# Optimization experiments

Hardware: AMD Instinct MI355X
Metric: run time of the kernel (lower is better)

Reference implementation:

```python
import jax, jax.numpy as jnp
import numpy as np

NUM_HEAD = 16
DIM = 1024
T, B = 2048, 4


def setup_inputs() -> dict:
    key = jax.random.key(0)
    ks = jax.random.split(key, 12)
    s = 1.0 / np.sqrt(DIM)
    return {
        "x1": jax.random.normal(ks[0], (T, B, DIM), jnp.float32),
        "x2": jax.random.normal(ks[1], (T, B, DIM), jnp.float32),
        "Wq": jax.random.normal(ks[2], (DIM, DIM), jnp.float32) * s,
        "bq": jax.random.normal(ks[3], (DIM,), jnp.float32) * 0.01,
        "Wk": jax.random.normal(ks[4], (DIM, DIM), jnp.float32) * s,
        "bk": jax.random.normal(ks[5], (DIM,), jnp.float32) * 0.01,
        "Wv": jax.random.normal(ks[6], (DIM, DIM), jnp.float32) * s,
        "bv": jax.random.normal(ks[7], (DIM,), jnp.float32) * 0.01,
        "Wu": jax.random.normal(ks[8], (DIM, DIM), jnp.float32) * s,
        "bu": jax.random.normal(ks[9], (DIM,), jnp.float32) * 0.01,
    }


def reference(x1, x2, Wq, bq, Wk, bk, Wv, bv, Wu, bu):
    T1, B1, C = x1.shape
    T2 = x2.shape[0]
    H = NUM_HEAD
    hd = C // H
    # (T,B,C) -> (B,T,C)
    x1b = jnp.transpose(x1, (1, 0, 2))
    x2b = jnp.transpose(x2, (1, 0, 2))
    # torch Linear: y = x @ W.T + b
    q = (x1b @ Wq.T + bq).reshape(B1, T1, H, hd).transpose(0, 2, 1, 3)  # (B,H,T1,hd)
    k = (x2b @ Wk.T + bk).reshape(B1, T2, H, hd).transpose(0, 2, 1, 3)
    v = (x2b @ Wv.T + bv).reshape(B1, T2, H, hd).transpose(0, 2, 1, 3)
    # NOTE: source scales by 1/sqrt(C) (full dim), not 1/sqrt(head_dim)
    attn = jnp.einsum("bhqd,bhkd->bhqk", q, k) / jnp.sqrt(jnp.asarray(C, q.dtype))
    attn = jax.nn.softmax(attn, axis=-1)
    # dropout = identity (eval mode, deterministic reference)
    out = jnp.einsum("bhqk,bhkd->bhqd", attn, v)  # (B,H,T1,hd)
    out = out.transpose(0, 2, 1, 3).reshape(B1, T1, C)  # merge heads
    out = out @ Wu.T + bu
    return out
```

## Files before the change

### kernel.cpp

```cpp
#include <hip/hip_runtime.h>

#define TSEQ 2048
#define BB 4
#define CDIM 1024
#define NH 16
#define HD 64
#define MR (TSEQ*BB)
#define C2SCALE 0.045084220f

typedef __attribute__((ext_vector_type(8))) short sh8;
typedef __attribute__((ext_vector_type(4))) short sh4;
typedef __attribute__((ext_vector_type(4))) float f4;

__device__ __forceinline__ unsigned short f2bf(float x){
  unsigned u = __builtin_bit_cast(unsigned, x);
  u += 0x7fffu + ((u>>16)&1u);
  return (unsigned short)(u>>16);
}

__device__ __forceinline__ unsigned pk2(float a, float b){
  unsigned ua = __builtin_bit_cast(unsigned, a) + 0x8000u;
  unsigned ub = __builtin_bit_cast(unsigned, b) + 0x8000u;
  return __builtin_amdgcn_perm(ua, ub, 0x07060302u);
}

__device__ __forceinline__ void gll16(const unsigned short* g, unsigned short* l){
  __builtin_amdgcn_global_load_lds(
      (const __attribute__((address_space(1))) unsigned int*)g,
      (__attribute__((address_space(3))) unsigned int*)l, 16, 0, 0);
}

__global__ void conv_x(const float* __restrict__ a, const float* __restrict__ b,
                       unsigned short* __restrict__ ya, unsigned short* __restrict__ yb){
  const float* s = blockIdx.y ? b : a;
  unsigned short* d = blockIdx.y ? yb : ya;
  int i = (blockIdx.x*256 + threadIdx.x)*4;
  f4 v = *(const f4*)(s+i);
  sh4 o;
  o.x = (short)f2bf(v.x); o.y = (short)f2bf(v.y);
  o.z = (short)f2bf(v.z); o.w = (short)f2bf(v.w);
  *(sh4*)(d+i) = o;
}

__global__ void conv_w(const float* __restrict__ w0, const float* __restrict__ w1,
                       const float* __restrict__ w2, const float* __restrict__ w3,
                       unsigned short* __restrict__ y0, unsigned short* __restrict__ y1,
                       unsigned short* __restrict__ y2, unsigned short* __restrict__ y3){
  const float* s; unsigned short* d;
  switch(blockIdx.y){
    case 0: s=w0; d=y0; break;
    case 1: s=w1; d=y1; break;
    case 2: s=w2; d=y2; break;
    default: s=w3; d=y3; break;
  }
  int i = (blockIdx.x*256 + threadIdx.x)*4;
  f4 v = *(const f4*)(s+i);
  sh4 o;
  o.x = (short)f2bf(v.x); o.y = (short)f2bf(v.y);
  o.z = (short)f2bf(v.z); o.w = (short)f2bf(v.w);
  *(sh4*)(d+i) = o;
}

template<int MODE>
__global__ __launch_bounds__(256,2) void gemm_bt(
    const unsigned short* __restrict__ A, const unsigned short* __restrict__ Bw,
    const float* __restrict__ bias, void* __restrict__ Cout){
  __shared__ unsigned short As[128*32];
  __shared__ unsigned short Bs[128*32];
  const int tid  = threadIdx.x;
  const int wave = tid>>6, lane = tid&63;
  const int g = lane>>4, c = lane&15;
  const int m0 = blockIdx.x*128, n0 = blockIdx.y*128;
  const int wr = wave>>1, wc = wave&1;
  f4 acc[4][4] = {};
  const int r0 = tid>>2, cc0 = tid&3;
  const unsigned short* Ag = A  + (size_t)(m0+r0)*CDIM + cc0*8;
  const unsigned short* Bg = Bw + (size_t)(n0+r0)*CDIM + cc0*8;

  for (int k0=0; k0<CDIM; k0+=32){
    __syncthreads();
    gll16(Ag + k0,                    As + tid*8);
    gll16(Ag + (size_t)64*CDIM + k0,  As + (256+tid)*8);
    gll16(Bg + k0,                    Bs + tid*8);
    gll16(Bg + (size_t)64*CDIM + k0,  Bs + (256+tid)*8);
    __syncthreads();
    sh8 af[4], bfr[4];
#pragma unroll
    for (int mt=0; mt<4; mt++) af[mt]  = *(const sh8*)(As + (wr*64+mt*16+c)*32 + g*8);
#pragma unroll
    for (int nt=0; nt<4; nt++) bfr[nt] = *(const sh8*)(Bs + (wc*64+nt*16+c)*32 + g*8);
#pragma unroll
    for (int mt=0; mt<4; mt++)
#pragma unroll
      for (int nt=0; nt<4; nt++)
        acc[mt][nt] = __builtin_amdgcn_mfma_f32_16x16x32_bf16(af[mt], bfr[nt], acc[mt][nt], 0,0,0);
  }

#pragma unroll
  for (int nt=0; nt<4; nt++){
    int nn = n0 + wc*64 + nt*16 + c;
    float bsv = bias[nn];
#pragma unroll
    for (int mt=0; mt<4; mt++){
      int mb = m0 + wr*64 + mt*16 + 4*g;
#pragma unroll
      for (int r=0; r<4; r++){
        float v = acc[mt][nt][r] + bsv;
        int mm = mb + r;
        if (MODE==3){
          ((unsigned short*)Cout)[(size_t)mm*CDIM + nn] = f2bf(v*C2SCALE);
        } else {
          ((float*)Cout)[(size_t)mm*CDIM + nn] = v;
        }
      }
    }
  }
}

__global__ __launch_bounds__(256,2) void gemm_kv(
    const unsigned short* __restrict__ A,
    const unsigned short* __restrict__ Bk, const unsigned short* __restrict__ Bv,
    const float* __restrict__ biask, const float* __restrict__ biasv,
    unsigned short* __restrict__ Kout, unsigned short* __restrict__ Vout){
  __shared__ unsigned short As[128*32];
  __shared__ unsigned short Bs1[128*32];
  __shared__ unsigned short Bs2[128*32];
  const int tid  = threadIdx.x;
  const int wave = tid>>6, lane = tid&63;
  const int g = lane>>4, c = lane&15;
  const int m0 = blockIdx.x*128, n0 = blockIdx.y*128;
  const int wr = wave>>1, wc = wave&1;
  f4 acck[4][4] = {}, accv[4][4] = {};
  const int r0 = tid>>2, cc0 = tid&3;
  const unsigned short* Ag  = A  + (size_t)(m0+r0)*CDIM + cc0*8;
  const unsigned short* Bkg = Bk + (size_t)(n0+r0)*CDIM + cc0*8;
  const unsigned short* Bvg = Bv + (size_t)(n0+r0)*CDIM + cc0*8;

  for (int k0=0; k0<CDIM; k0+=32){
    __syncthreads();
    gll16(Ag  + k0,                    As  + tid*8);
    gll16(Ag  + (size_t)64*CDIM + k0,  As  + (256+tid)*8);
    gll16(Bkg + k0,                    Bs1 + tid*8);
    gll16(Bkg + (size_t)64*CDIM + k0,  Bs1 + (256+tid)*8);
    gll16(Bvg + k0,                    Bs2 + tid*8);
    gll16(Bvg + (size_t)64*CDIM + k0,  Bs2 + (256+tid)*8);
    __syncthreads();
    sh8 af[4], bk4[4], bv4[4];
#pragma unroll
    for (int mt=0; mt<4; mt++) af[mt]  = *(const sh8*)(As  + (wr*64+mt*16+c)*32 + g*8);
#pragma unroll
    for (int nt=0; nt<4; nt++) bk4[nt] = *(const sh8*)(Bs1 + (wc*64+nt*16+c)*32 + g*8);
#pragma unroll
    for (int nt=0; nt<4; nt++) bv4[nt] = *(const sh8*)(Bs2 + (wc*64+nt*16+c)*32 + g*8);
#pragma unroll
    for (int mt=0; mt<4; mt++)
#pragma unroll
      for (int nt=0; nt<4; nt++){
        acck[mt][nt] = __builtin_amdgcn_mfma_f32_16x16x32_bf16(af[mt], bk4[nt], acck[mt][nt], 0,0,0);
        accv[mt][nt] = __builtin_amdgcn_mfma_f32_16x16x32_bf16(af[mt], bv4[nt], accv[mt][nt], 0,0,0);
      }
  }

#pragma unroll
  for (int nt=0; nt<4; nt++){
    int nn = n0 + wc*64 + nt*16 + c;
    float bkv = biask[nn], bvv = biasv[nn];
#pragma unroll
    for (int mt=0; mt<4; mt++){
      int mb = m0 + wr*64 + mt*16 + 4*g;
#pragma unroll
      for (int r=0; r<4; r++){
        int mm = mb + r;
        Kout[(size_t)mm*CDIM + nn] = f2bf(acck[mt][nt][r] + bkv);
        int t = mm>>2, bb = mm&3, h = nn>>6, d = nn&63;
        Vout[(((size_t)bb*NH + h)*HD + d)*TSEQ + t] = f2bf(accv[mt][nt][r] + bvv);
      }
    }
  }
}

__global__ __launch_bounds__(256,3) void attn_kernel(
    const unsigned short* __restrict__ Q, const unsigned short* __restrict__ Kb,
    const unsigned short* __restrict__ Vt, unsigned short* __restrict__ O){
  __shared__ unsigned short Ks[128*64];
  __shared__ unsigned short Vs[64*128];
  __shared__ unsigned short Ps[4][32*64];
  const int tid=threadIdx.x, wave=tid>>6, lane=tid&63;
  const int g=lane>>4, c=lane&15;
  const int gx = blockIdx.x;
  const int bh = ((gx>>7)<<3) | (gx&7);
  const int qt = (gx>>3)&15;
  const int b = bh>>4, h = bh&15;
  const int qbase = qt*128 + wave*32;

  sh8 qfr[2][2];
#pragma unroll
  for (int qf=0; qf<2; qf++)
#pragma unroll
    for (int kc=0; kc<2; kc++){
      int t = qbase + qf*16 + c;
      qfr[qf][kc] = *(const sh8*)(Q + ((size_t)t*BB + b)*CDIM + h*HD + kc*32 + g*8);
    }

  f4 oacc[4][2] = {};
  float lrun[2] = {0.f, 0.f};

  for (int k0=0; k0<TSEQ; k0+=128){
    __syncthreads();
#pragma unroll
    for (int i=0; i<4; i++){
      int cc = i*256+tid, row = cc>>3, ch = (cc&7) ^ (row&7);
      gll16(Kb + ((size_t)(k0+row)*BB + b)*CDIM + h*HD + ch*8, Ks + cc*8);
    }
#pragma unroll
    for (int i=0; i<4; i++){
      int cc = i*256+tid, d = cc>>4, ch = (cc&15) ^ (d&15);
      gll16(Vt + ((size_t)(b*NH+h)*HD + d)*TSEQ + k0 + ch*8, Vs + cc*8);
    }
    __syncthreads();

    f4 sacc[8][2] = {};
#pragma unroll
    for (int kf=0; kf<8; kf++){
      sh8 af[2];
#pragma unroll
      for (int kc=0; kc<2; kc++){
        int ch = (kc*4+g) ^ (c&7);
        af[kc] = *(const sh8*)(Ks + (kf*16+c)*64 + ch*8);
      }
#pragma unroll
      for (int kc=0; kc<2; kc++)
#pragma unroll
        for (int qf=0; qf<2; qf++)
          sacc[kf][qf] = __builtin_amdgcn_mfma_f32_16x16x32_bf16(af[kc], qfr[qf][kc], sacc[kf][qf],0,0,0);
    }

#pragma unroll
    for (int half=0; half<2; half++){
#pragma unroll
      for (int qf=0; qf<2; qf++){
        unsigned short* prow = Ps[wave] + (qf*16+c)*64;
#pragma unroll
        for (int kfl=0; kfl<4; kfl++){
          int kf = half*4 + kfl;
          float p0 = __builtin_amdgcn_exp2f(sacc[kf][qf][0]);
          float p1 = __builtin_amdgcn_exp2f(sacc[kf][qf][1]);
          float p2 = __builtin_amdgcn_exp2f(sacc[kf][qf][2]);
          float p3 = __builtin_amdgcn_exp2f(sacc[kf][qf][3]);
          lrun[qf] += (p0+p1)+(p2+p3);
          unsigned d0 = pk2(p1, p0);
          unsigned d1 = pk2(p3, p2);
          int js = (kfl*4+g) ^ (c&14);
          uint2 pr; pr.x = d0; pr.y = d1;
          *(uint2*)(prow + js*4) = pr;
        }
      }
#pragma unroll
      for (int kc2l=0; kc2l<2; kc2l++){
        int kc2 = half*2 + kc2l;
        sh8 pf[2];
#pragma unroll
        for (int qf=0; qf<2; qf++){
          int j0 = kc2l*8 + 2*g;
          pf[qf] = *(const sh8*)(Ps[wave] + (qf*16+c)*64 + ((j0 ^ (c&14)))*4);
        }
#pragma unroll
        for (int df=0; df<4; df++){
          int ch = (kc2*4+g) ^ c;
          sh8 vf = *(const sh8*)(Vs + (df*16+c)*128 + ch*8);
#pragma unroll
          for (int qf=0; qf<2; qf++)
            oacc[df][qf] = __builtin_amdgcn_mfma_f32_16x16x32_bf16(vf, pf[qf], oacc[df][qf],0,0,0);
        }
      }
    }
  }

#pragma unroll
  for (int qf=0; qf<2; qf++){
    lrun[qf] += __shfl_xor(lrun[qf], 16, 64);
    lrun[qf] += __shfl_xor(lrun[qf], 32, 64);
    float inv = 1.0f/lrun[qf];
    int t = qbase + qf*16 + c;
#pragma unroll
    for (int df=0; df<4; df++){
      uint2 pr;
      pr.x = pk2(oacc[df][qf][1]*inv, oacc[df][qf][0]*inv);
      pr.y = pk2(oacc[df][qf][3]*inv, oacc[df][qf][2]*inv);
      *(uint2*)(O + ((size_t)b*TSEQ + t)*CDIM + h*HD + df*16 + 4*g) = pr;
    }
  }
}

extern "C" void kernel_launch(void* const* d_in, const int* in_sizes, int n_in,
                              void* d_out, int out_size, void* d_ws, size_t ws_size,
                              hipStream_t stream){
  (void)in_sizes; (void)n_in; (void)out_size; (void)ws_size;
  const float* x1 = (const float*)d_in[0];
  const float* x2 = (const float*)d_in[1];
  const float* Wq = (const float*)d_in[2];
  const float* bq = (const float*)d_in[3];
  const float* Wk = (const float*)d_in[4];
  const float* bk = (const float*)d_in[5];
  const float* Wv = (const float*)d_in[6];
  const float* bv = (const float*)d_in[7];
  const float* Wu = (const float*)d_in[8];
  const float* bu = (const float*)d_in[9];

  unsigned short* ws = (unsigned short*)d_ws;
  size_t o = 0;
  unsigned short* x1b = ws + o; o += (size_t)MR*CDIM;
  unsigned short* x2b = ws + o; o += (size_t)MR*CDIM;
  unsigned short* wqb = ws + o; o += (size_t)CDIM*CDIM;
  unsigned short* wkb = ws + o; o += (size_t)CDIM*CDIM;
  unsigned short* wvb = ws + o; o += (size_t)CDIM*CDIM;
  unsigned short* wub = ws + o; o += (size_t)CDIM*CDIM;
  unsigned short* Qb  = ws + o; o += (size_t)MR*CDIM;
  unsigned short* Kbf = ws + o; o += (size_t)MR*CDIM;
  unsigned short* Vtb = ws + o; o += (size_t)MR*CDIM;
  unsigned short* Ob  = x1b;

  conv_x<<<dim3((MR*CDIM)/1024, 2),   256, 0, stream>>>(x1, x2, x1b, x2b);
  conv_w<<<dim3((CDIM*CDIM)/1024, 4), 256, 0, stream>>>(Wq, Wk, Wv, Wu, wqb, wkb, wvb, wub);

  dim3 gg(MR/128, CDIM/128);
  gemm_bt<3><<<gg, 256, 0, stream>>>(x1b, wqb, bq, Qb);
  gemm_kv  <<<gg, 256, 0, stream>>>(x2b, wkb, wvb, bk, bv, Kbf, Vtb);
  attn_kernel<<<dim3(1024), 256, 0, stream>>>(Qb, Kbf, Vtb, Ob);
  gemm_bt<2><<<gg, 256, 0, stream>>>(Ob, wub, bu, (float*)d_out);
}
```

Measured before the change: 374.3 us.

## Merge Q/K/V projections into one launch and register-prefetch K/V tiles in attention

The Q projection and the fused K/V projection become a single gemm_qkv launch over a 3-deep grid z-dimension, each block computing one projection, which cuts a launch and gives more parallel blocks. The attention kernel switches from direct global-to-LDS loads to register prefetch: the next K/V tile is loaded into registers while the current tile is computed, then written to LDS after a barrier. This overlaps global loads with MFMA work, at the cost of more registers (which may lower occupancy under launch bounds of 3) and an extra barrier per iteration. The K/V split also drops the reuse of the shared x2 A-tile that the old fused K/V kernel had.

```diff
diff --git a/kernel.cpp b/kernel.cpp
--- a/kernel.cpp
+++ b/kernel.cpp
@@ -61,10 +61,9 @@
   *(sh4*)(d+i) = o;
 }
 
-template<int MODE>
-__global__ __launch_bounds__(256,2) void gemm_bt(
+__global__ __launch_bounds__(256,2) void gemm_u(
     const unsigned short* __restrict__ A, const unsigned short* __restrict__ Bw,
-    const float* __restrict__ bias, void* __restrict__ Cout){
+    const float* __restrict__ bias, float* __restrict__ Cout){
   __shared__ unsigned short As[128*32];
   __shared__ unsigned short Bs[128*32];
   const int tid  = threadIdx.x;
@@ -104,76 +103,73 @@
     for (int mt=0; mt<4; mt++){
       int mb = m0 + wr*64 + mt*16 + 4*g;
 #pragma unroll
-      for (int r=0; r<4; r++){
-        float v = acc[mt][nt][r] + bsv;
-        int mm = mb + r;
-        if (MODE==3){
-          ((unsigned short*)Cout)[(size_t)mm*CDIM + nn] = f2bf(v*C2SCALE);
-        } else {
-          ((float*)Cout)[(size_t)mm*CDIM + nn] = v;
-        }
-      }
-    }
-  }
-}
-
-__global__ __launch_bounds__(256,2) void gemm_kv(
-    const unsigned short* __restrict__ A,
-    const unsigned short* __restrict__ Bk, const unsigned short* __restrict__ Bv,
-    const float* __restrict__ biask, const float* __restrict__ biasv,
-    unsigned short* __restrict__ Kout, unsigned short* __restrict__ Vout){
+      for (int r=0; r<4; r++)
+        Cout[(size_t)(mb+r)*CDIM + nn] = acc[mt][nt][r] + bsv;
+    }
+  }
+}
+
+__global__ __launch_bounds__(256,2) void gemm_qkv(
+    const unsigned short* __restrict__ x1b, const unsigned short* __restrict__ x2b,
+    const unsigned short* __restrict__ wq, const unsigned short* __restrict__ wk,
+    const unsigned short* __restrict__ wv,
+    const float* __restrict__ bq, const float* __restrict__ bk, const float* __restrict__ bv,
+    unsigned short* __restrict__ Qo, unsigned short* __restrict__ Ko,
+    unsigned short* __restrict__ Vo){
   __shared__ unsigned short As[128*32];
-  __shared__ unsigned short Bs1[128*32];
-  __shared__ unsigned short Bs2[128*32];
+  __shared__ unsigned short Bs[128*32];
+  const int z = blockIdx.z;
+  const unsigned short* A  = (z==0) ? x1b : x2b;
+  const unsigned short* Bw = (z==0) ? wq : (z==1) ? wk : wv;
+  const float* bias        = (z==0) ? bq : (z==1) ? bk : bv;
   const int tid  = threadIdx.x;
   const int wave = tid>>6, lane = tid&63;
   const int g = lane>>4, c = lane&15;
   const int m0 = blockIdx.x*128, n0 = blockIdx.y*128;
   const int wr = wave>>1, wc = wave&1;
-  f4 acck[4][4] = {}, accv[4][4] = {};
+  f4 acc[4][4] = {};
   const int r0 = tid>>2, cc0 = tid&3;
-  const unsigned short* Ag  = A  + (size_t)(m0+r0)*CDIM + cc0*8;
-  const unsigned short* Bkg = Bk + (size_t)(n0+r0)*CDIM + cc0*8;
-  const unsigned short* Bvg = Bv + (size_t)(n0+r0)*CDIM + cc0*8;
+  const unsigned short* Ag = A  + (size_t)(m0+r0)*CDIM + cc0*8;
+  const unsigned short* Bg = Bw + (size_t)(n0+r0)*CDIM + cc0*8;
 
   for (int k0=0; k0<CDIM; k0+=32){
     __syncthreads();
-    gll16(Ag  + k0,                    As  + tid*8);
-    gll16(Ag  + (size_t)64*CDIM + k0,  As  + (256+tid)*8);
-    gll16(Bkg + k0,                    Bs1 + tid*8);
-    gll16(Bkg + (size_t)64*CDIM + k0,  Bs1 + (256+tid)*8);
-    gll16(Bvg + k0,                    Bs2 + tid*8);
-    gll16(Bvg + (size_t)64*CDIM + k0,  Bs2 + (256+tid)*8);
-    __syncthreads();
-    sh8 af[4], bk4[4], bv4[4];
-#pragma unroll
-    for (int mt=0; mt<4; mt++) af[mt]  = *(const sh8*)(As  + (wr*64+mt*16+c)*32 + g*8);
-#pragma unroll
-    for (int nt=0; nt<4; nt++) bk4[nt] = *(const sh8*)(Bs1 + (wc*64+nt*16+c)*32 + g*8);
-#pragma unroll
-    for (int nt=0; nt<4; nt++) bv4[nt] = *(const sh8*)(Bs2 + (wc*64+nt*16+c)*32 + g*8);
+    gll16(Ag + k0,                    As + tid*8);
+    gll16(Ag + (size_t)64*CDIM + k0,  As + (256+tid)*8);
+    gll16(Bg + k0,                    Bs + tid*8);
+    gll16(Bg + (size_t)64*CDIM + k0,  Bs + (256+tid)*8);
+    __syncthreads();
+    sh8 af[4], bfr[4];
+#pragma unroll
+    for (int mt=0; mt<4; mt++) af[mt]  = *(const sh8*)(As + (wr*64+mt*16+c)*32 + g*8);
+#pragma unroll
+    for (int nt=0; nt<4; nt++) bfr[nt] = *(const sh8*)(Bs + (wc*64+nt*16+c)*32 + g*8);
 #pragma unroll
     for (int mt=0; mt<4; mt++)
 #pragma unroll
-      for (int nt=0; nt<4; nt++){
-        acck[mt][nt] = __builtin_amdgcn_mfma_f32_16x16x32_bf16(af[mt], bk4[nt], acck[mt][nt], 0,0,0);
-        accv[mt][nt] = __builtin_amdgcn_mfma_f32_16x16x32_bf16(af[mt], bv4[nt], accv[mt][nt], 0,0,0);
-      }
+      for (int nt=0; nt<4; nt++)
+        acc[mt][nt] = __builtin_amdgcn_mfma_f32_16x16x32_bf16(af[mt], bfr[nt], acc[mt][nt], 0,0,0);
   }
 
 #pragma unroll
   for (int nt=0; nt<4; nt++){
     int nn = n0 + wc*64 + nt*16 + c;
-    float bkv = biask[nn], bvv = biasv[nn];
+    float bsv = bias[nn];
 #pragma unroll
     for (int mt=0; mt<4; mt++){
       int mb = m0 + wr*64 + mt*16 + 4*g;
 #pragma unroll
       for (int r=0; r<4; r++){
+        float v = acc[mt][nt][r] + bsv;
         int mm = mb + r;
-        Kout[(size_t)mm*CDIM + nn] = f2bf(acck[mt][nt][r] + bkv);
-        int t = mm>>2, bb = mm&3, h = nn>>6, d = nn&63;
-        Vout[(((size_t)bb*NH + h)*HD + d)*TSEQ + t] = f2bf(accv[mt][nt][r] + bvv);
+        if (z==0){
+          Qo[(size_t)mm*CDIM + nn] = f2bf(v*C2SCALE);
+        } else if (z==1){
+          Ko[(size_t)mm*CDIM + nn] = f2bf(v);
+        } else {
+          int t = mm>>2, bb = mm&3, h = nn>>6, d = nn&63;
+          Vo[(((size_t)bb*NH + h)*HD + d)*TSEQ + t] = f2bf(v);
+        }
       }
     }
   }
@@ -193,6 +189,17 @@
   const int b = bh>>4, h = bh&15;
   const int qbase = qt*128 + wave*32;
 
+  const unsigned short* kbase[4];
+  const unsigned short* vbase[4];
+#pragma unroll
+  for (int i=0; i<4; i++){
+    int cc = i*256+tid;
+    int krow = cc>>3, kch = (cc&7) ^ (krow&7);
+    kbase[i] = Kb + ((size_t)krow*BB + b)*CDIM + h*HD + kch*8;
+    int vd = cc>>4, vch = (cc&15) ^ (vd&15);
+    vbase[i] = Vt + ((size_t)(b*NH+h)*HD + vd)*TSEQ + vch*8;
+  }
+
   sh8 qfr[2][2];
 #pragma unroll
   for (int qf=0; qf<2; qf++)
@@ -205,19 +212,28 @@
   f4 oacc[4][2] = {};
   float lrun[2] = {0.f, 0.f};
 
-  for (int k0=0; k0<TSEQ; k0+=128){
-    __syncthreads();
-#pragma unroll
-    for (int i=0; i<4; i++){
-      int cc = i*256+tid, row = cc>>3, ch = (cc&7) ^ (row&7);
-      gll16(Kb + ((size_t)(k0+row)*BB + b)*CDIM + h*HD + ch*8, Ks + cc*8);
-    }
-#pragma unroll
-    for (int i=0; i<4; i++){
-      int cc = i*256+tid, d = cc>>4, ch = (cc&15) ^ (d&15);
-      gll16(Vt + ((size_t)(b*NH+h)*HD + d)*TSEQ + k0 + ch*8, Vs + cc*8);
-    }
-    __syncthreads();
+  f4 kreg[4], vreg[4];
+#pragma unroll
+  for (int i=0; i<4; i++){
+    kreg[i] = *(const f4*)(kbase[i]);
+    vreg[i] = *(const f4*)(vbase[i]);
+  }
+#pragma unroll
+  for (int i=0; i<4; i++){
+    *(f4*)(Ks + (i*256+tid)*8) = kreg[i];
+    *(f4*)(Vs + (i*256+tid)*8) = vreg[i];
+  }
+  __syncthreads();
+
+  for (int iter=0; iter<TSEQ/128; iter++){
+    if (iter < TSEQ/128-1){
+      int k0n = (iter+1)*128;
+#pragma unroll
+      for (int i=0; i<4; i++){
+        kreg[i] = *(const f4*)(kbase[i] + (size_t)k0n*BB*CDIM);
+        vreg[i] = *(const f4*)(vbase[i] + k0n);
+      }
+    }
 
     f4 sacc[8][2] = {};
 #pragma unroll
@@ -248,10 +264,8 @@
           float p2 = __builtin_amdgcn_exp2f(sacc[kf][qf][2]);
           float p3 = __builtin_amdgcn_exp2f(sacc[kf][qf][3]);
           lrun[qf] += (p0+p1)+(p2+p3);
-          unsigned d0 = pk2(p1, p0);
-          unsigned d1 = pk2(p3, p2);
+          uint2 pr; pr.x = pk2(p1, p0); pr.y = pk2(p3, p2);
           int js = (kfl*4+g) ^ (c&14);
-          uint2 pr; pr.x = d0; pr.y = d1;
           *(uint2*)(prow + js*4) = pr;
         }
       }
@@ -273,6 +287,16 @@
             oacc[df][qf] = __builtin_amdgcn_mfma_f32_16x16x32_bf16(vf, pf[qf], oacc[df][qf],0,0,0);
         }
       }
+    }
+
+    __syncthreads();
+    if (iter < TSEQ/128-1){
+#pragma unroll
+      for (int i=0; i<4; i++){
+        *(f4*)(Ks + (i*256+tid)*8) = kreg[i];
+        *(f4*)(Vs + (i*256+tid)*8) = vreg[i];
+      }
+      __syncthreads();
     }
   }
 
@@ -323,9 +347,8 @@
   conv_x<<<dim3((MR*CDIM)/1024, 2),   256, 0, stream>>>(x1, x2, x1b, x2b);
   conv_w<<<dim3((CDIM*CDIM)/1024, 4), 256, 0, stream>>>(Wq, Wk, Wv, Wu, wqb, wkb, wvb, wub);
 
-  dim3 gg(MR/128, CDIM/128);
-  gemm_bt<3><<<gg, 256, 0, stream>>>(x1b, wqb, bq, Qb);
-  gemm_kv  <<<gg, 256, 0, stream>>>(x2b, wkb, wvb, bk, bv, Kbf, Vtb);
+  gemm_qkv<<<dim3(MR/128, CDIM/128, 3), 256, 0, stream>>>(
+      x1b, x2b, wqb, wkb, wvb, bq, bk, bv, Qb, Kbf, Vtb);
   attn_kernel<<<dim3(1024), 256, 0, stream>>>(Qb, Kbf, Vtb, Ob);
-  gemm_bt<2><<<gg, 256, 0, stream>>>(Ob, wub, bu, (float*)d_out);
-}
+  gemm_u<<<dim3(MR/128, CDIM/128), 256, 0, stream>>>(Ob, wub, bu, (float*)d_out);
+}
```

After: 357.0 us. 4.6% less time.
